# Kernel tuning notes

Hardware: AMD Instinct MI355X
Metric: run time of the kernel (lower is better)

## Reference

```python
import jax, jax.numpy as jnp
import numpy as np

B = 262144
SLOPE = 0.2

def _xavier(key, shape):
    # shape = (out_ch, in_ch, k); fan_in = in_ch*k, fan_out = out_ch*k
    fan_in = shape[1] * shape[2]
    fan_out = shape[0] * shape[2]
    limit = np.sqrt(6.0 / (fan_in + fan_out)).astype(np.float32)
    return jax.random.uniform(key, shape, jnp.float32, -limit, limit)

def setup_inputs() -> dict:
    key = jax.random.key(0)
    ks = jax.random.split(key, 5)
    x = jax.random.normal(ks[0], (B, 2, 16), jnp.float32)
    return {
        "x": x,
        "w_enc1": _xavier(ks[1], (4, 2, 3)), "b_enc1": jnp.zeros((4,), jnp.float32),
        "w_bneck": _xavier(ks[2], (8, 4, 3)), "b_bneck": jnp.zeros((8,), jnp.float32),
        "w_dec1": _xavier(ks[3], (4, 8, 3)), "b_dec1": jnp.zeros((4,), jnp.float32),
        "w_out": _xavier(ks[4], (2, 4, 3)), "b_out": jnp.zeros((2,), jnp.float32),
    }

def _conv1d(x, w, b, stride):
    # x: [B, C_in, L], w: [C_out, C_in, K], padding=1
    y = jax.lax.conv_general_dilated(
        x, w, window_strides=(stride,), padding=[(1, 1)],
        dimension_numbers=("NCH", "OIH", "NCH"))
    return y + b[None, :, None]

def _leaky(y):
    return jnp.where(y > 0, y, SLOPE * y)

def _upsample2(y):
    # nearest-neighbor x2 along length
    return jnp.repeat(y, 2, axis=-1)

def reference(x, w_enc1, b_enc1, w_bneck, b_bneck, w_dec1, b_dec1, w_out, b_out):
    enc1 = _leaky(_conv1d(x, w_enc1, b_enc1, 2))          # [B,4,8]
    bneck = _leaky(_conv1d(enc1, w_bneck, b_bneck, 2))    # [B,8,4]
    up1 = _upsample2(bneck)                               # [B,8,8]
    dec1 = _leaky(_conv1d(up1, w_dec1, b_dec1, 1))        # [B,4,8]
    skip = dec1 + enc1                                    # [B,4,8]
    up2 = _upsample2(skip)                                # [B,4,16]
    out = jnp.tanh(_conv1d(up2, w_out, b_out, 1))         # [B,2,16]
    return out
```

## Files before the change

### kernel.cpp

```cpp
#include <hip/hip_runtime.h>

#define SLOPE 0.2f

__device__ __forceinline__ float leaky(float v) {
    return v > 0.0f ? v : SLOPE * v;
}

__device__ __forceinline__ float fast_tanh(float v) {
    float e = __expf(2.0f * v);
    return 1.0f - 2.0f * __builtin_amdgcn_rcpf(e + 1.0f);
}

__global__ __launch_bounds__(256) void minigen_kernel(
    const float* __restrict__ x,
    const float* __restrict__ w1, const float* __restrict__ b1,
    const float* __restrict__ w2, const float* __restrict__ b2,
    const float* __restrict__ w3, const float* __restrict__ b3,
    const float* __restrict__ w4, const float* __restrict__ b4,
    float* __restrict__ out, int n)
{
    int i = blockIdx.x * blockDim.x + threadIdx.x;
    if (i >= n) return;

    float xr[32];
    const float4* xin = (const float4*)(x + (size_t)i * 32);
#pragma unroll
    for (int q = 0; q < 8; ++q) {
        float4 v = xin[q];
        xr[4*q+0] = v.x; xr[4*q+1] = v.y; xr[4*q+2] = v.z; xr[4*q+3] = v.w;
    }

    float e1[4][8];
#pragma unroll
    for (int oc = 0; oc < 4; ++oc) {
#pragma unroll
        for (int ol = 0; ol < 8; ++ol) {
            float s = b1[oc];
#pragma unroll
            for (int ic = 0; ic < 2; ++ic) {
#pragma unroll
                for (int k = 0; k < 3; ++k) {
                    int j = 2*ol - 1 + k;
                    if (j >= 0 && j < 16)
                        s += xr[ic*16 + j] * w1[(oc*2 + ic)*3 + k];
                }
            }
            e1[oc][ol] = leaky(s);
        }
    }

    float bn[8][4];
#pragma unroll
    for (int oc = 0; oc < 8; ++oc) {
#pragma unroll
        for (int ol = 0; ol < 4; ++ol) {
            float s = b2[oc];
#pragma unroll
            for (int ic = 0; ic < 4; ++ic) {
#pragma unroll
                for (int k = 0; k < 3; ++k) {
                    int j = 2*ol - 1 + k;
                    if (j >= 0 && j < 8)
                        s += e1[ic][j] * w2[(oc*4 + ic)*3 + k];
                }
            }
            bn[oc][ol] = leaky(s);
        }
    }

    float sk[4][8];
#pragma unroll
    for (int oc = 0; oc < 4; ++oc) {
#pragma unroll
        for (int ol = 0; ol < 8; ++ol) {
            float s = b3[oc];
#pragma unroll
            for (int ic = 0; ic < 8; ++ic) {
#pragma unroll
                for (int k = 0; k < 3; ++k) {
                    int j = ol - 1 + k;
                    if (j >= 0 && j < 8)
                        s += bn[ic][j >> 1] * w3[(oc*8 + ic)*3 + k];
                }
            }
            sk[oc][ol] = leaky(s) + e1[oc][ol];
        }
    }

    float o[32];
#pragma unroll
    for (int oc = 0; oc < 2; ++oc) {
#pragma unroll
        for (int ol = 0; ol < 16; ++ol) {
            float s = b4[oc];
#pragma unroll
            for (int ic = 0; ic < 4; ++ic) {
#pragma unroll
                for (int k = 0; k < 3; ++k) {
                    int j = ol - 1 + k;
                    if (j >= 0 && j < 16)
                        s += sk[ic][j >> 1] * w4[(oc*4 + ic)*3 + k];
                }
            }
            o[oc*16 + ol] = fast_tanh(s);
        }
    }

    float4* op = (float4*)(out + (size_t)i * 32);
#pragma unroll
    for (int q = 0; q < 8; ++q) {
        op[q] = make_float4(o[4*q+0], o[4*q+1], o[4*q+2], o[4*q+3]);
    }
}

extern "C" void kernel_launch(void* const* d_in, const int* in_sizes, int n_in,
                              void* d_out, int out_size, void* d_ws, size_t ws_size,
                              hipStream_t stream) {
    const float* x  = (const float*)d_in[0];
    const float* w1 = (const float*)d_in[1];
    const float* b1 = (const float*)d_in[2];
    const float* w2 = (const float*)d_in[3];
    const float* b2 = (const float*)d_in[4];
    const float* w3 = (const float*)d_in[5];
    const float* b3 = (const float*)d_in[6];
    const float* w4 = (const float*)d_in[7];
    const float* b4 = (const float*)d_in[8];
    float* out = (float*)d_out;

    int n = in_sizes[0] / 32;
    const int block = 256;
    int grid = (n + block - 1) / block;
    hipLaunchKernelGGL(minigen_kernel, dim3(grid), dim3(block), 0, stream,
                       x, w1, b1, w2, b2, w3, b3, w4, b4, out, n);
}
```

Measured before the change: 120.1 us.

## Stage input and output through padded LDS for coalesced global access

Loads each block's 256 samples into shared memory with fully coalesced float4 reads, and each thread then pulls its own 32 floats from a row padded to 9 float4s to avoid bank conflicts. Outputs go back through the same LDS buffer so the global writes are coalesced too. Before this, each thread read and wrote 128 contiguous bytes, so every wave instruction touched strided addresses. It also uses explicit fmaf and a max-based leaky ReLU, in exchange for 36KB of LDS per block and two block barriers, which may reduce occupancy.

```diff
diff --git a/kernel.cpp b/kernel.cpp
--- a/kernel.cpp
+++ b/kernel.cpp
@@ -3,7 +3,7 @@
 #define SLOPE 0.2f
 
 __device__ __forceinline__ float leaky(float v) {
-    return v > 0.0f ? v : SLOPE * v;
+    return __builtin_fmaxf(v, SLOPE * v);
 }
 
 __device__ __forceinline__ float fast_tanh(float v) {
@@ -19,97 +19,126 @@
     const float* __restrict__ w4, const float* __restrict__ b4,
     float* __restrict__ out, int n)
 {
-    int i = blockIdx.x * blockDim.x + threadIdx.x;
-    if (i >= n) return;
+    __shared__ float4 lds[256 * 9];
+
+    const int t = threadIdx.x;
+    const int sample = blockIdx.x * 256 + t;
+    const long long f4total = (long long)n * 8;
+    const long long blockBase = (long long)blockIdx.x * 2048;
+
+    const float4* xin = (const float4*)x;
+#pragma unroll
+    for (int q = 0; q < 8; ++q) {
+        int g = q * 256 + t;
+        if (blockBase + g < f4total) {
+            float4 v = xin[blockBase + g];
+            int s = g >> 3, r = g & 7;
+            lds[s * 9 + r] = v;
+        }
+    }
+    __syncthreads();
 
     float xr[32];
-    const float4* xin = (const float4*)(x + (size_t)i * 32);
 #pragma unroll
-    for (int q = 0; q < 8; ++q) {
-        float4 v = xin[q];
-        xr[4*q+0] = v.x; xr[4*q+1] = v.y; xr[4*q+2] = v.z; xr[4*q+3] = v.w;
-    }
-
-    float e1[4][8];
-#pragma unroll
-    for (int oc = 0; oc < 4; ++oc) {
-#pragma unroll
-        for (int ol = 0; ol < 8; ++ol) {
-            float s = b1[oc];
-#pragma unroll
-            for (int ic = 0; ic < 2; ++ic) {
-#pragma unroll
-                for (int k = 0; k < 3; ++k) {
-                    int j = 2*ol - 1 + k;
-                    if (j >= 0 && j < 16)
-                        s += xr[ic*16 + j] * w1[(oc*2 + ic)*3 + k];
-                }
-            }
-            e1[oc][ol] = leaky(s);
-        }
-    }
-
-    float bn[8][4];
-#pragma unroll
-    for (int oc = 0; oc < 8; ++oc) {
-#pragma unroll
-        for (int ol = 0; ol < 4; ++ol) {
-            float s = b2[oc];
-#pragma unroll
-            for (int ic = 0; ic < 4; ++ic) {
-#pragma unroll
-                for (int k = 0; k < 3; ++k) {
-                    int j = 2*ol - 1 + k;
-                    if (j >= 0 && j < 8)
-                        s += e1[ic][j] * w2[(oc*4 + ic)*3 + k];
-                }
-            }
-            bn[oc][ol] = leaky(s);
-        }
-    }
-
-    float sk[4][8];
-#pragma unroll
-    for (int oc = 0; oc < 4; ++oc) {
-#pragma unroll
-        for (int ol = 0; ol < 8; ++ol) {
-            float s = b3[oc];
-#pragma unroll
-            for (int ic = 0; ic < 8; ++ic) {
-#pragma unroll
-                for (int k = 0; k < 3; ++k) {
-                    int j = ol - 1 + k;
-                    if (j >= 0 && j < 8)
-                        s += bn[ic][j >> 1] * w3[(oc*8 + ic)*3 + k];
-                }
-            }
-            sk[oc][ol] = leaky(s) + e1[oc][ol];
-        }
+    for (int r = 0; r < 8; ++r) {
+        float4 v = lds[t * 9 + r];
+        xr[4*r+0] = v.x; xr[4*r+1] = v.y; xr[4*r+2] = v.z; xr[4*r+3] = v.w;
     }
 
     float o[32];
+    if (sample < n) {
+        float e1[4][8];
 #pragma unroll
-    for (int oc = 0; oc < 2; ++oc) {
+        for (int oc = 0; oc < 4; ++oc) {
 #pragma unroll
-        for (int ol = 0; ol < 16; ++ol) {
-            float s = b4[oc];
+            for (int ol = 0; ol < 8; ++ol) {
+                float s = b1[oc];
 #pragma unroll
-            for (int ic = 0; ic < 4; ++ic) {
+                for (int ic = 0; ic < 2; ++ic) {
 #pragma unroll
-                for (int k = 0; k < 3; ++k) {
-                    int j = ol - 1 + k;
-                    if (j >= 0 && j < 16)
-                        s += sk[ic][j >> 1] * w4[(oc*4 + ic)*3 + k];
+                    for (int k = 0; k < 3; ++k) {
+                        int j = 2*ol - 1 + k;
+                        if (j >= 0 && j < 16)
+                            s = fmaf(xr[ic*16 + j], w1[(oc*2 + ic)*3 + k], s);
+                    }
                 }
+                e1[oc][ol] = leaky(s);
             }
-            o[oc*16 + ol] = fast_tanh(s);
         }
+
+        float bn[8][4];
+#pragma unroll
+        for (int oc = 0; oc < 8; ++oc) {
+#pragma unroll
+            for (int ol = 0; ol < 4; ++ol) {
+                float s = b2[oc];
+#pragma unroll
+                for (int ic = 0; ic < 4; ++ic) {
+#pragma unroll
+                    for (int k = 0; k < 3; ++k) {
+                        int j = 2*ol - 1 + k;
+                        if (j >= 0 && j < 8)
+                            s = fmaf(e1[ic][j], w2[(oc*4 + ic)*3 + k], s);
+                    }
+                }
+                bn[oc][ol] = leaky(s);
+            }
+        }
+
+        float sk[4][8];
+#pragma unroll
+        for (int oc = 0; oc < 4; ++oc) {
+#pragma unroll
+            for (int ol = 0; ol < 8; ++ol) {
+                float s = b3[oc];
+#pragma unroll
+                for (int ic = 0; ic < 8; ++ic) {
+#pragma unroll
+                    for (int k = 0; k < 3; ++k) {
+                        int j = ol - 1 + k;
+                        if (j >= 0 && j < 8)
+                            s = fmaf(bn[ic][j >> 1], w3[(oc*8 + ic)*3 + k], s);
+                    }
+                }
+                sk[oc][ol] = leaky(s) + e1[oc][ol];
+            }
+        }
+
+#pragma unroll
+        for (int oc = 0; oc < 2; ++oc) {
+#pragma unroll
+            for (int ol = 0; ol < 16; ++ol) {
+                float s = b4[oc];
+#pragma unroll
+                for (int ic = 0; ic < 4; ++ic) {
+#pragma unroll
+                    for (int k = 0; k < 3; ++k) {
+                        int j = ol - 1 + k;
+                        if (j >= 0 && j < 16)
+                            s = fmaf(sk[ic][j >> 1], w4[(oc*4 + ic)*3 + k], s);
+                    }
+                }
+                o[oc*16 + ol] = fast_tanh(s);
+            }
+        }
+    } else {
+#pragma unroll
+        for (int q = 0; q < 32; ++q) o[q] = 0.0f;
     }
 
-    float4* op = (float4*)(out + (size_t)i * 32);
+#pragma unroll
+    for (int r = 0; r < 8; ++r)
+        lds[t * 9 + r] = make_float4(o[4*r+0], o[4*r+1], o[4*r+2], o[4*r+3]);
+    __syncthreads();
+
+    float4* op = (float4*)out;
 #pragma unroll
     for (int q = 0; q < 8; ++q) {
-        op[q] = make_float4(o[4*q+0], o[4*q+1], o[4*q+2], o[4*q+3]);
+        int g = q * 256 + t;
+        if (blockBase + g < f4total) {
+            int s = g >> 3, r = g & 7;
+            op[blockBase + g] = lds[s * 9 + r];
+        }
     }
 }
 
```

Measured after the change: 107.2 us. 1.12x faster.

## Split each sample across two lanes with DPP halo exchange and LDS-staged coalesced IO

Applied to the files above, without the earlier changes.

Each sample is now processed by a pair of lanes, each computing half of the length dimension. The lanes swap boundary (halo) values with DPP quad-permutes. Input and output go through padded LDS tiles so global loads and stores are fully coalesced float4 accesses instead of per-thread 128-byte strided ones. Leaky ReLU becomes fmax, and launch bounds request higher occupancy. The tail-bound check is dropped, so it assumes n is a multiple of 128, and it adds LDS use and two barriers.

```diff
diff --git a/kernel.cpp b/kernel.cpp
--- a/kernel.cpp
+++ b/kernel.cpp
@@ -3,7 +3,7 @@
 #define SLOPE 0.2f
 
 __device__ __forceinline__ float leaky(float v) {
-    return v > 0.0f ? v : SLOPE * v;
+    return __builtin_fmaxf(v, SLOPE * v);
 }
 
 __device__ __forceinline__ float fast_tanh(float v) {
@@ -11,105 +11,159 @@
     return 1.0f - 2.0f * __builtin_amdgcn_rcpf(e + 1.0f);
 }
 
-__global__ __launch_bounds__(256) void minigen_kernel(
+__device__ __forceinline__ float swap1(float v) {
+    int i = __builtin_bit_cast(int, v);
+    i = __builtin_amdgcn_mov_dpp(i, 0xB1, 0xF, 0xF, true);
+    return __builtin_bit_cast(float, i);
+}
+
+__global__ __launch_bounds__(256, 6) void minigen_kernel(
     const float* __restrict__ x,
     const float* __restrict__ w1, const float* __restrict__ b1,
     const float* __restrict__ w2, const float* __restrict__ b2,
     const float* __restrict__ w3, const float* __restrict__ b3,
     const float* __restrict__ w4, const float* __restrict__ b4,
-    float* __restrict__ out, int n)
+    float* __restrict__ out)
 {
-    int i = blockIdx.x * blockDim.x + threadIdx.x;
-    if (i >= n) return;
+    __shared__ float4 lds[128 * 9];
 
-    float xr[32];
-    const float4* xin = (const float4*)(x + (size_t)i * 32);
+    const int t = threadIdx.x;
+    const int p = t & 1;
+    const int row = t >> 1;
+    const long long blockBase = (long long)blockIdx.x * 1024;
+
+    const float4* xin = (const float4*)x;
 #pragma unroll
-    for (int q = 0; q < 8; ++q) {
-        float4 v = xin[q];
-        xr[4*q+0] = v.x; xr[4*q+1] = v.y; xr[4*q+2] = v.z; xr[4*q+3] = v.w;
+    for (int q = 0; q < 4; ++q) {
+        int g = q * 256 + t;
+        float4 v = xin[blockBase + g];
+        lds[(g >> 3) * 9 + (g & 7)] = v;
+    }
+    __syncthreads();
+
+    float xr[2][8];
+#pragma unroll
+    for (int ic = 0; ic < 2; ++ic) {
+#pragma unroll
+        for (int m = 0; m < 2; ++m) {
+            float4 v = lds[row * 9 + ic * 4 + p * 2 + m];
+            xr[ic][4*m+0] = v.x; xr[ic][4*m+1] = v.y;
+            xr[ic][4*m+2] = v.z; xr[ic][4*m+3] = v.w;
+        }
     }
 
-    float e1[4][8];
+    float xw[2][9];
+#pragma unroll
+    for (int ic = 0; ic < 2; ++ic) {
+        float h = swap1(xr[ic][7]);
+        xw[ic][0] = p ? h : 0.0f;
+#pragma unroll
+        for (int j = 0; j < 8; ++j) xw[ic][j+1] = xr[ic][j];
+    }
+    float e1h[4][4];
 #pragma unroll
     for (int oc = 0; oc < 4; ++oc) {
 #pragma unroll
-        for (int ol = 0; ol < 8; ++ol) {
+        for (int l = 0; l < 4; ++l) {
             float s = b1[oc];
 #pragma unroll
-            for (int ic = 0; ic < 2; ++ic) {
+            for (int ic = 0; ic < 2; ++ic)
 #pragma unroll
-                for (int k = 0; k < 3; ++k) {
-                    int j = 2*ol - 1 + k;
-                    if (j >= 0 && j < 16)
-                        s += xr[ic*16 + j] * w1[(oc*2 + ic)*3 + k];
-                }
-            }
-            e1[oc][ol] = leaky(s);
+                for (int k = 0; k < 3; ++k)
+                    s = fmaf(xw[ic][2*l + k], w1[(oc*2 + ic)*3 + k], s);
+            e1h[oc][l] = leaky(s);
         }
     }
 
-    float bn[8][4];
+    float ew[4][5];
+#pragma unroll
+    for (int ic = 0; ic < 4; ++ic) {
+        float h = swap1(e1h[ic][3]);
+        ew[ic][0] = p ? h : 0.0f;
+#pragma unroll
+        for (int j = 0; j < 4; ++j) ew[ic][j+1] = e1h[ic][j];
+    }
+    float bnh[8][2];
 #pragma unroll
     for (int oc = 0; oc < 8; ++oc) {
 #pragma unroll
-        for (int ol = 0; ol < 4; ++ol) {
+        for (int l = 0; l < 2; ++l) {
             float s = b2[oc];
 #pragma unroll
-            for (int ic = 0; ic < 4; ++ic) {
+            for (int ic = 0; ic < 4; ++ic)
 #pragma unroll
-                for (int k = 0; k < 3; ++k) {
-                    int j = 2*ol - 1 + k;
-                    if (j >= 0 && j < 8)
-                        s += e1[ic][j] * w2[(oc*4 + ic)*3 + k];
-                }
-            }
-            bn[oc][ol] = leaky(s);
+                for (int k = 0; k < 3; ++k)
+                    s = fmaf(ew[ic][2*l + k], w2[(oc*4 + ic)*3 + k], s);
+            bnh[oc][l] = leaky(s);
         }
     }
 
-    float sk[4][8];
+    float bw[8][6];
+#pragma unroll
+    for (int ic = 0; ic < 8; ++ic) {
+        float hR = swap1(bnh[ic][0]);
+        float hL = swap1(bnh[ic][1]);
+        bw[ic][0] = p ? hL : 0.0f;
+        bw[ic][1] = bnh[ic][0]; bw[ic][2] = bnh[ic][0];
+        bw[ic][3] = bnh[ic][1]; bw[ic][4] = bnh[ic][1];
+        bw[ic][5] = p ? 0.0f : hR;
+    }
+    float skh[4][4];
 #pragma unroll
     for (int oc = 0; oc < 4; ++oc) {
 #pragma unroll
-        for (int ol = 0; ol < 8; ++ol) {
+        for (int l = 0; l < 4; ++l) {
             float s = b3[oc];
 #pragma unroll
-            for (int ic = 0; ic < 8; ++ic) {
+            for (int ic = 0; ic < 8; ++ic)
 #pragma unroll
-                for (int k = 0; k < 3; ++k) {
-                    int j = ol - 1 + k;
-                    if (j >= 0 && j < 8)
-                        s += bn[ic][j >> 1] * w3[(oc*8 + ic)*3 + k];
-                }
-            }
-            sk[oc][ol] = leaky(s) + e1[oc][ol];
+                for (int k = 0; k < 3; ++k)
+                    s = fmaf(bw[ic][l + k], w3[(oc*8 + ic)*3 + k], s);
+            skh[oc][l] = leaky(s) + e1h[oc][l];
         }
     }
 
-    float o[32];
+    float sw[4][10];
+#pragma unroll
+    for (int ic = 0; ic < 4; ++ic) {
+        float hL = swap1(skh[ic][3]);
+        float hR = swap1(skh[ic][0]);
+        sw[ic][0] = p ? hL : 0.0f;
+        sw[ic][1] = skh[ic][0]; sw[ic][2] = skh[ic][0];
+        sw[ic][3] = skh[ic][1]; sw[ic][4] = skh[ic][1];
+        sw[ic][5] = skh[ic][2]; sw[ic][6] = skh[ic][2];
+        sw[ic][7] = skh[ic][3]; sw[ic][8] = skh[ic][3];
+        sw[ic][9] = p ? 0.0f : hR;
+    }
+    float oh[2][8];
 #pragma unroll
     for (int oc = 0; oc < 2; ++oc) {
 #pragma unroll
-        for (int ol = 0; ol < 16; ++ol) {
+        for (int l = 0; l < 8; ++l) {
             float s = b4[oc];
 #pragma unroll
-            for (int ic = 0; ic < 4; ++ic) {
+            for (int ic = 0; ic < 4; ++ic)
 #pragma unroll
-                for (int k = 0; k < 3; ++k) {
-                    int j = ol - 1 + k;
-                    if (j >= 0 && j < 16)
-                        s += sk[ic][j >> 1] * w4[(oc*4 + ic)*3 + k];
-                }
-            }
-            o[oc*16 + ol] = fast_tanh(s);
+                for (int k = 0; k < 3; ++k)
+                    s = fmaf(sw[ic][l + k], w4[(oc*4 + ic)*3 + k], s);
+            oh[oc][l] = fast_tanh(s);
         }
     }
 
-    float4* op = (float4*)(out + (size_t)i * 32);
 #pragma unroll
-    for (int q = 0; q < 8; ++q) {
-        op[q] = make_float4(o[4*q+0], o[4*q+1], o[4*q+2], o[4*q+3]);
+    for (int oc = 0; oc < 2; ++oc)
+#pragma unroll
+        for (int m = 0; m < 2; ++m)
+            lds[row * 9 + oc * 4 + p * 2 + m] =
+                make_float4(oh[oc][4*m+0], oh[oc][4*m+1],
+                            oh[oc][4*m+2], oh[oc][4*m+3]);
+    __syncthreads();
+
+    float4* op = (float4*)out;
+#pragma unroll
+    for (int q = 0; q < 4; ++q) {
+        int g = q * 256 + t;
+        op[blockBase + g] = lds[(g >> 3) * 9 + (g & 7)];
     }
 }
 
@@ -128,8 +182,7 @@
     float* out = (float*)d_out;
 
     int n = in_sizes[0] / 32;
-    const int block = 256;
-    int grid = (n + block - 1) / block;
-    hipLaunchKernelGGL(minigen_kernel, dim3(grid), dim3(block), 0, stream,
-                       x, w1, b1, w2, b2, w3, b3, w4, b4, out, n);
+    int grid = n / 128;
+    hipLaunchKernelGGL(minigen_kernel, dim3(grid), dim3(256), 0, stream,
+                       x, w1, b1, w2, b2, w3, b3, w4, b4, out);
 }
```

Result: faster. 106.8 us (-11.0%).

## Stage input/output through padded LDS for coalesced loads and use packed v2f FMAs

Applied to the files above, without the earlier changes.

Input and output tiles are now staged through padded shared memory, so global float4 accesses become fully coalesced across the block instead of each thread striding 128 bytes. The conv arithmetic is rewritten to compute output-channel pairs with packed two-wide FMAs, and leaky ReLU becomes a vector max. Launch bounds add a minimum occupancy hint, and the bounds check is removed on the assumption that n is a multiple of 256. The cost is two barriers plus about 36KB of LDS per block, which may limit occupancy.

```diff
diff --git a/kernel.cpp b/kernel.cpp
--- a/kernel.cpp
+++ b/kernel.cpp
@@ -1,115 +1,156 @@
 #include <hip/hip_runtime.h>
+
+typedef float v2f __attribute__((ext_vector_type(2)));
 
 #define SLOPE 0.2f
 
-__device__ __forceinline__ float leaky(float v) {
-    return v > 0.0f ? v : SLOPE * v;
+static __device__ __forceinline__ v2f leaky2(v2f v) {
+    return __builtin_elementwise_max(v, SLOPE * v);
 }
 
-__device__ __forceinline__ float fast_tanh(float v) {
+static __device__ __forceinline__ v2f fma2(v2f a, v2f b, v2f c) {
+    return __builtin_elementwise_fma(a, b, c);
+}
+
+static __device__ __forceinline__ float fast_tanh(float v) {
     float e = __expf(2.0f * v);
     return 1.0f - 2.0f * __builtin_amdgcn_rcpf(e + 1.0f);
 }
 
-__global__ __launch_bounds__(256) void minigen_kernel(
+__global__ __launch_bounds__(256, 4) void minigen_kernel(
     const float* __restrict__ x,
     const float* __restrict__ w1, const float* __restrict__ b1,
     const float* __restrict__ w2, const float* __restrict__ b2,
     const float* __restrict__ w3, const float* __restrict__ b3,
     const float* __restrict__ w4, const float* __restrict__ b4,
-    float* __restrict__ out, int n)
+    float* __restrict__ out)
 {
-    int i = blockIdx.x * blockDim.x + threadIdx.x;
-    if (i >= n) return;
+    __shared__ float4 lds[256 * 9];
 
-    float xr[32];
-    const float4* xin = (const float4*)(x + (size_t)i * 32);
+    const int t = threadIdx.x;
+    const int blockBase = blockIdx.x * 2048;
+
+    const float4* xin = (const float4*)x;
 #pragma unroll
     for (int q = 0; q < 8; ++q) {
-        float4 v = xin[q];
-        xr[4*q+0] = v.x; xr[4*q+1] = v.y; xr[4*q+2] = v.z; xr[4*q+3] = v.w;
+        int g = q * 256 + t;
+        lds[(g >> 3) * 9 + (g & 7)] = xin[blockBase + g];
+    }
+    __syncthreads();
+
+    float xr[2][16];
+#pragma unroll
+    for (int m = 0; m < 8; ++m) {
+        float4 v = lds[t * 9 + m];
+        int c = m >> 2, base = (m & 3) * 4;
+        xr[c][base+0] = v.x; xr[c][base+1] = v.y;
+        xr[c][base+2] = v.z; xr[c][base+3] = v.w;
     }
 
-    float e1[4][8];
+    v2f e1p[2][8];
 #pragma unroll
-    for (int oc = 0; oc < 4; ++oc) {
+    for (int cp = 0; cp < 2; ++cp) {
 #pragma unroll
-        for (int ol = 0; ol < 8; ++ol) {
-            float s = b1[oc];
+        for (int l = 0; l < 8; ++l) {
+            v2f s = { b1[2*cp], b1[2*cp+1] };
 #pragma unroll
-            for (int ic = 0; ic < 2; ++ic) {
+            for (int ic = 0; ic < 2; ++ic)
 #pragma unroll
                 for (int k = 0; k < 3; ++k) {
-                    int j = 2*ol - 1 + k;
-                    if (j >= 0 && j < 16)
-                        s += xr[ic*16 + j] * w1[(oc*2 + ic)*3 + k];
+                    int u = 2*l - 1 + k;
+                    if (u >= 0) {
+                        v2f w = { w1[((2*cp)*2 + ic)*3 + k],
+                                  w1[((2*cp+1)*2 + ic)*3 + k] };
+                        float xv = xr[ic][u];
+                        s = fma2(w, (v2f){xv, xv}, s);
+                    }
                 }
-            }
-            e1[oc][ol] = leaky(s);
+            e1p[cp][l] = leaky2(s);
         }
     }
 
-    float bn[8][4];
+    v2f bnp[4][4];
 #pragma unroll
-    for (int oc = 0; oc < 8; ++oc) {
+    for (int cp = 0; cp < 4; ++cp) {
 #pragma unroll
-        for (int ol = 0; ol < 4; ++ol) {
-            float s = b2[oc];
+        for (int l = 0; l < 4; ++l) {
+            v2f s = { b2[2*cp], b2[2*cp+1] };
 #pragma unroll
-            for (int ic = 0; ic < 4; ++ic) {
+            for (int ic = 0; ic < 4; ++ic)
 #pragma unroll
                 for (int k = 0; k < 3; ++k) {
-                    int j = 2*ol - 1 + k;
-                    if (j >= 0 && j < 8)
-                        s += e1[ic][j] * w2[(oc*4 + ic)*3 + k];
+                    int u = 2*l - 1 + k;
+                    if (u >= 0) {
+                        float ev = (ic & 1) ? e1p[ic>>1][u].y
+                                            : e1p[ic>>1][u].x;
+                        v2f w = { w2[((2*cp)*4 + ic)*3 + k],
+                                  w2[((2*cp+1)*4 + ic)*3 + k] };
+                        s = fma2(w, (v2f){ev, ev}, s);
+                    }
                 }
-            }
-            bn[oc][ol] = leaky(s);
+            bnp[cp][l] = leaky2(s);
         }
     }
 
-    float sk[4][8];
+    v2f skp[2][8];
 #pragma unroll
-    for (int oc = 0; oc < 4; ++oc) {
+    for (int cp = 0; cp < 2; ++cp) {
 #pragma unroll
-        for (int ol = 0; ol < 8; ++ol) {
-            float s = b3[oc];
+        for (int l = 0; l < 8; ++l) {
+            v2f s = { b3[2*cp], b3[2*cp+1] };
 #pragma unroll
-            for (int ic = 0; ic < 8; ++ic) {
+            for (int ic = 0; ic < 8; ++ic)
 #pragma unroll
                 for (int k = 0; k < 3; ++k) {
-                    int j = ol - 1 + k;
-                    if (j >= 0 && j < 8)
-                        s += bn[ic][j >> 1] * w3[(oc*8 + ic)*3 + k];
+                    int u = l - 1 + k;
+                    if (u >= 0 && u < 8) {
+                        int j = u >> 1;
+                        float bv = (ic & 1) ? bnp[ic>>1][j].y
+                                            : bnp[ic>>1][j].x;
+                        v2f w = { w3[((2*cp)*8 + ic)*3 + k],
+                                  w3[((2*cp+1)*8 + ic)*3 + k] };
+                        s = fma2(w, (v2f){bv, bv}, s);
+                    }
                 }
-            }
-            sk[oc][ol] = leaky(s) + e1[oc][ol];
+            skp[cp][l] = leaky2(s) + e1p[cp][l];
         }
     }
 
-    float o[32];
+    v2f op4[16];
 #pragma unroll
-    for (int oc = 0; oc < 2; ++oc) {
+    for (int l = 0; l < 16; ++l) {
+        v2f s = { b4[0], b4[1] };
 #pragma unroll
-        for (int ol = 0; ol < 16; ++ol) {
-            float s = b4[oc];
+        for (int ic = 0; ic < 4; ++ic)
 #pragma unroll
-            for (int ic = 0; ic < 4; ++ic) {
-#pragma unroll
-                for (int k = 0; k < 3; ++k) {
-                    int j = ol - 1 + k;
-                    if (j >= 0 && j < 16)
-                        s += sk[ic][j >> 1] * w4[(oc*4 + ic)*3 + k];
+            for (int k = 0; k < 3; ++k) {
+                int u = l - 1 + k;
+                if (u >= 0 && u < 16) {
+                    int j = u >> 1;
+                    float sv = (ic & 1) ? skp[ic>>1][j].y
+                                        : skp[ic>>1][j].x;
+                    v2f w = { w4[(0*4 + ic)*3 + k],
+                              w4[(1*4 + ic)*3 + k] };
+                    s = fma2(w, (v2f){sv, sv}, s);
                 }
             }
-            o[oc*16 + ol] = fast_tanh(s);
-        }
+        op4[l] = (v2f){ fast_tanh(s.x), fast_tanh(s.y) };
     }
 
-    float4* op = (float4*)(out + (size_t)i * 32);
+#pragma unroll
+    for (int m = 0; m < 4; ++m) {
+        lds[t*9 + m]     = make_float4(op4[4*m+0].x, op4[4*m+1].x,
+                                       op4[4*m+2].x, op4[4*m+3].x);
+        lds[t*9 + 4 + m] = make_float4(op4[4*m+0].y, op4[4*m+1].y,
+                                       op4[4*m+2].y, op4[4*m+3].y);
+    }
+    __syncthreads();
+
+    float4* outp = (float4*)out;
 #pragma unroll
     for (int q = 0; q < 8; ++q) {
-        op[q] = make_float4(o[4*q+0], o[4*q+1], o[4*q+2], o[4*q+3]);
+        int g = q * 256 + t;
+        outp[blockBase + g] = lds[(g >> 3) * 9 + (g & 7)];
     }
 }
 
@@ -128,8 +169,7 @@
     float* out = (float*)d_out;
 
     int n = in_sizes[0] / 32;
-    const int block = 256;
-    int grid = (n + block - 1) / block;
-    hipLaunchKernelGGL(minigen_kernel, dim3(grid), dim3(block), 0, stream,
-                       x, w1, b1, w2, b2, w3, b3, w4, b4, out, n);
+    int grid = n / 256;
+    hipLaunchKernelGGL(minigen_kernel, dim3(grid), dim3(256), 0, stream,
+                       x, w1, b1, w2, b2, w3, b3, w4, b4, out);
 }
```

Result: faster. 104.8 us (-12.7%).
